# Optimization experiments

Measured on AMD Instinct MI355X. Metric: run time of the kernel, lower is better.

The kernel has to match this reference:

```python
import jax, jax.numpy as jnp
import numpy as np


def setup_inputs() -> dict:
    key = jax.random.key(0)
    ks = jax.random.split(key, 12)
    B, C, H, W = 8, 256, 64, 64
    inter = C // 8
    s = 0.05  # weight scale keeps q.k logits in a stable softmax range
    f32 = jnp.float32
    x = jax.random.normal(ks[0], (B, C, H, W), f32)
    Wq = jax.random.normal(ks[1], (inter, C), f32) * s
    bq = jnp.zeros((inter,), f32)
    Wk = jax.random.normal(ks[2], (inter, C), f32) * s
    bk = jnp.zeros((inter,), f32)
    Wv = jax.random.normal(ks[3], (C, C), f32) * s
    bv = jnp.zeros((C,), f32)
    gamma = jnp.full((1,), 0.5, f32)  # learnable residual scale (init 0 in torch; 0.5 exercises the path)
    Wg1 = jax.random.normal(ks[4], (inter, C), f32) * s
    bg1 = jnp.zeros((inter,), f32)
    Wg2 = jax.random.normal(ks[5], (C, inter), f32) * s
    bg2 = jnp.zeros((C,), f32)
    return {"x": x, "Wq": Wq, "bq": bq, "Wk": Wk, "bk": bk, "Wv": Wv, "bv": bv,
            "gamma": gamma, "Wg1": Wg1, "bg1": bg1, "Wg2": Wg2, "bg2": bg2}


def reference(x, Wq, bq, Wk, bk, Wv, bv, gamma, Wg1, bg1, Wg2, bg2):
    B, C, H, W = x.shape
    N = H * W
    xf = x.reshape(B, C, N)  # [B,C,N]
    # 1x1 convs == per-pixel linear projections
    q = jnp.einsum('oc,bcn->bon', Wq, xf) + bq[None, :, None]  # [B,inter,N]
    k = jnp.einsum('oc,bcn->bon', Wk, xf) + bk[None, :, None]  # [B,inter,N]
    v = jnp.einsum('oc,bcn->bon', Wv, xf) + bv[None, :, None]  # [B,C,N]
    # attention[b,n,m] = softmax_m( q[b,:,n] . k[b,:,m] )
    attn = jax.nn.softmax(jnp.einsum('bin,bim->bnm', q, k), axis=-1)  # [B,N,N]
    # out[b,c,n] = sum_m v[b,c,m] * attn[b,n,m]
    out = jnp.einsum('bcm,bnm->bcn', v, attn)  # [B,C,N]
    out = gamma[0] * out + xf
    # gated global pooling branch: GAP -> 1x1 conv -> ReLU -> 1x1 conv -> Sigmoid
    gp = xf.mean(axis=-1)  # [B,C]
    h = jax.nn.relu(jnp.einsum('oc,bc->bo', Wg1, gp) + bg1)  # [B,inter]
    ga = jax.nn.sigmoid(jnp.einsum('co,bo->bc', Wg2, h) + bg2)  # [B,C]
    out = out * ga[:, :, None] + out
    return out.reshape(B, C, H, W)
```

## Files before the change

kernel.cpp:

```cpp
#include <hip/hip_runtime.h>

typedef unsigned short u16;
typedef unsigned int   u32;
typedef short s16x4 __attribute__((ext_vector_type(4)));
typedef u16 u16x4 __attribute__((ext_vector_type(4)));
typedef u16 u16x8 __attribute__((ext_vector_type(8)));
typedef __bf16 bf16x8 __attribute__((ext_vector_type(8)));
typedef float f32x4 __attribute__((ext_vector_type(4)));

#define NB 8
#define NC 256
#define NI 32
#define NN 4096
#define LOG2E 1.4426950408889634f
#define POFF 64.0f

#define OW_Q   0
#define OB_Q   8192
#define OW_K   8224
#define OB_K   16416
#define OW_V   16448
#define OB_V   81984
#define OGAM   82240
#define OW_G1  82248
#define OB_G1  90440
#define OW_G2  90472
#define OB_G2  98664
#define WTOT   98920

__device__ __forceinline__ float bf2f(u16 v) {
    u32 u = ((u32)v) << 16;
    return __builtin_bit_cast(float, u);
}
__device__ __forceinline__ u16 f2bf(float f) {
    u32 u = __builtin_bit_cast(u32, f);
    u32 lsb = (u >> 16) & 1u;
    u += 0x7fffu + lsb;
    return (u16)(u >> 16);
}
__device__ __forceinline__ bool is_f32_mode(const void* graw) {
    return ((const u16*)graw)[0] == 0;
}

__global__ __launch_bounds__(256) void convert_kernel(
    const void* x,  const void* Wq, const void* bq, const void* Wk, const void* bk,
    const void* Wv, const void* bv, const void* gamma, const void* Wg1, const void* bg1,
    const void* Wg2, const void* bg2, float* __restrict__ xf, float* __restrict__ wbuf,
    u16* __restrict__ wbf, float* __restrict__ gp)
{
    bool f32m = is_f32_mode(gamma);
    int blk = blockIdx.x, t = threadIdx.x;
    if (blk < 2048) {
        int base = blk * 4096 + t * 16;
        float s = 0.f;
        if (f32m) {
            const float* xs = (const float*)x;
#pragma unroll
            for (int k = 0; k < 4; ++k) {
                f32x4 a = *(const f32x4*)(xs + base + k * 4);
                s += (a[0] + a[1]) + (a[2] + a[3]);
            }
        } else {
            const u16* xs = (const u16*)x;
#pragma unroll
            for (int k = 0; k < 2; ++k) {
                u16x8 a = *(const u16x8*)(xs + base + k * 8);
                f32x4 lo, hi;
#pragma unroll
                for (int j = 0; j < 4; ++j) { lo[j] = bf2f(a[j]); hi[j] = bf2f(a[4 + j]); }
                *(f32x4*)(xf + base + k * 8)     = lo;
                *(f32x4*)(xf + base + k * 8 + 4) = hi;
                s += (lo[0]+lo[1])+(lo[2]+lo[3]) + (hi[0]+hi[1])+(hi[2]+hi[3]);
            }
        }
#pragma unroll
        for (int off = 1; off <= 32; off <<= 1) s += __shfl_xor(s, off, 64);
        __shared__ float ws[4];
        if ((t & 63) == 0) ws[t >> 6] = s;
        __syncthreads();
        if (t == 0) gp[blk] = (ws[0] + ws[1] + ws[2] + ws[3]) * (1.0f / NN);
        return;
    }
    if (blk < 2080) {
        int tid = (blk - 2048) * 256 + t;
        const int off[12] = {OW_Q, OB_Q, OW_K, OB_K, OW_V, OB_V, OGAM, OW_G1, OB_G1, OW_G2, OB_G2, WTOT};
        const int len[11] = {8192, 32, 8192, 32, 65536, 256, 1, 8192, 32, 8192, 256};
        const void* srcs[11] = {Wq, bq, Wk, bk, Wv, bv, gamma, Wg1, bg1, Wg2, bg2};
        for (int w = tid; w < WTOT; w += 32 * 256) {
            int seg = 0;
#pragma unroll
            for (int i = 1; i < 11; ++i) if (w >= off[i]) seg = i;
            int idx = w - off[seg];
            float val = 0.f;
            if (idx < len[seg])
                val = f32m ? ((const float*)srcs[seg])[idx] : bf2f(((const u16*)srcs[seg])[idx]);
            wbuf[w] = val;
        }
        return;
    }
    int tid = (blk - 2080) * 256 + t;
    for (int w = tid; w < 320 * 256; w += 10 * 256) {
        int row = w >> 8, c = w & 255;
        const void* src; int idx; float scale = 1.f;
        if (row < 32)      { src = Wq; idx = row * 256 + c; scale = LOG2E; }
        else if (row < 64) { src = Wk; idx = (row - 32) * 256 + c; }
        else               { src = Wv; idx = (row - 64) * 256 + c; }
        float val = f32m ? ((const float*)src)[idx] : bf2f(((const u16*)src)[idx]);
        wbf[w] = f2bf(val * scale);
    }
}

__global__ __launch_bounds__(256) void proj_kernel(
    const void* xr, const float* __restrict__ xf, const void* graw,
    const float* __restrict__ wbuf, const u16* __restrict__ wbf,
    u16* __restrict__ qt, u16* __restrict__ kt, u16* __restrict__ v)
{
    __shared__ __attribute__((aligned(16))) u16 xs[64][264];

    const float* X = is_f32_mode(graw) ? (const float*)xr : xf;

    int t    = threadIdx.x;
    int lane = t & 63;
    int wave = t >> 6;
    int b    = blockIdx.x >> 6;
    int m0   = (blockIdx.x & 63) << 6;
    int l15  = lane & 15;
    int quad = lane >> 4;

    {
        const float* xb = X + (size_t)b * NC * NN + m0 + lane;
        int c0 = wave * 64;
#pragma unroll
        for (int ci = 0; ci < 64; ci += 4) {
            int c = c0 + ci;
            float a0 = xb[(size_t)(c    ) * NN];
            float a1 = xb[(size_t)(c + 1) * NN];
            float a2 = xb[(size_t)(c + 2) * NN];
            float a3 = xb[(size_t)(c + 3) * NN];
            u16x4 p4 = { f2bf(a0), f2bf(a1), f2bf(a2), f2bf(a3) };
            *(u16x4*)&xs[lane][c] = p4;
        }
    }
    __syncthreads();

    const f32x4 zero4 = {};
    f32x4 acc[5][4];
#pragma unroll
    for (int i = 0; i < 5; ++i)
#pragma unroll
        for (int mt = 0; mt < 4; ++mt) acc[i][mt] = zero4;

    int obase = wave * 80;
    const u16* wb = wbf + (size_t)(obase + l15) * 256 + quad * 8;

    bf16x8 af[5];
#pragma unroll
    for (int i = 0; i < 5; ++i)
        af[i] = *(const bf16x8*)(wb + (size_t)(i * 16) * 256);

#pragma unroll
    for (int kc = 0; kc < 8; ++kc) {
        bf16x8 afn[5], bfr[4];
        if (kc < 7) {
#pragma unroll
            for (int i = 0; i < 5; ++i)
                afn[i] = *(const bf16x8*)(wb + (size_t)(i * 16) * 256 + (kc + 1) * 32);
        }
#pragma unroll
        for (int mt = 0; mt < 4; ++mt)
            bfr[mt] = *(const bf16x8*)&xs[mt * 16 + l15][kc * 32 + quad * 8];
#pragma unroll
        for (int i = 0; i < 5; ++i)
#pragma unroll
            for (int mt = 0; mt < 4; ++mt)
                acc[i][mt] = __builtin_amdgcn_mfma_f32_16x16x32_bf16(af[i], bfr[mt], acc[i][mt], 0, 0, 0);
        if (kc < 7) {
#pragma unroll
            for (int i = 0; i < 5; ++i) af[i] = afn[i];
        }
    }

    __syncthreads();

    if (wave == 0) {
#pragma unroll
        for (int i = 0; i < 4; ++i) {
#pragma unroll
            for (int mt = 0; mt < 4; ++mt) {
                u16x4 tmp;
#pragma unroll
                for (int r = 0; r < 4; ++r) {
                    int o = i * 16 + quad * 4 + r;
                    float bias = (o < 32) ? LOG2E * wbuf[OB_Q + o] : wbuf[OB_K + o - 32];
                    tmp[r] = f2bf(acc[i][mt][r] + bias);
                }
                *(u16x4*)&xs[mt * 16 + l15][i * 16 + quad * 4] = tmp;
            }
        }
        int m = m0 + lane;
        u16* qrow = qt + (size_t)(b * NN + m) * NI;
        u16* krow = kt + (size_t)(b * NN + m) * NI;
#pragma unroll
        for (int j = 0; j < 4; ++j) *(u16x8*)(qrow + j * 8) = *(const u16x8*)&xs[lane][j * 8];
#pragma unroll
        for (int j = 0; j < 4; ++j) *(u16x8*)(krow + j * 8) = *(const u16x8*)&xs[lane][32 + j * 8];
#pragma unroll
        for (int mt = 0; mt < 4; ++mt) {
#pragma unroll
            for (int r = 0; r < 4; ++r) {
                int c = quad * 4 + r;
                v[(size_t)(b * NC + c) * NN + m0 + mt * 16 + l15] = f2bf(acc[4][mt][r] + wbuf[OB_V + c]);
            }
        }
    } else {
#pragma unroll
        for (int i = 0; i < 5; ++i) {
#pragma unroll
            for (int mt = 0; mt < 4; ++mt) {
#pragma unroll
                for (int r = 0; r < 4; ++r) {
                    int c = wave * 80 + i * 16 + quad * 4 + r - 64;
                    v[(size_t)(b * NC + c) * NN + m0 + mt * 16 + l15] = f2bf(acc[i][mt][r] + wbuf[OB_V + c]);
                }
            }
        }
    }
}

__global__ __launch_bounds__(256) void gate_kernel(
    const float* __restrict__ gp, const float* __restrict__ wbuf, float* __restrict__ gmul)
{
    int b = blockIdx.x;
    int t = threadIdx.x;
    __shared__ float gps[NC];
    __shared__ float hs[NI];
    gps[t] = gp[b * NC + t];
    __syncthreads();
    if (t < NI) {
        float a = wbuf[OB_G1 + t];
        for (int c = 0; c < NC; ++c) a += wbuf[OW_G1 + t * NC + c] * gps[c];
        hs[t] = a > 0.f ? a : 0.f;
    }
    __syncthreads();
    float a = wbuf[OB_G2 + t];
#pragma unroll
    for (int i = 0; i < NI; ++i) a += wbuf[OW_G2 + t * NI + i] * hs[i];
    float sig = 1.f / (1.f + __expf(-a));
    gmul[b * NC + t] = 1.f + sig;
}

__global__ __launch_bounds__(512, 4) void flash_kernel(
    const u16* __restrict__ qt, const u16* __restrict__ kt, const u16* __restrict__ v,
    const void* xr, const float* __restrict__ xf, const void* graw,
    const float* __restrict__ wbuf, const float* __restrict__ gmul, void* outp)
{
    __shared__ __attribute__((aligned(16))) u16 vs[2][NC][48];

    bool f32m = is_f32_mode(graw);
    const float* X = f32m ? (const float*)xr : xf;

    int t    = threadIdx.x;
    int lane = t & 63;
    int wave = t >> 6;
    int b    = blockIdx.x >> 6;
    int nblk = (blockIdx.x & 63) << 6;
    int n0   = nblk + (wave >> 2) * 32;
    int c0   = (wave & 3) * 64;
    int l15  = lane & 15;
    int quad = lane >> 4;

    const f32x4 zero4 = {};

    bf16x8 qf[2];
#pragma unroll
    for (int n16 = 0; n16 < 2; ++n16)
        qf[n16] = *(const bf16x8*)(qt + (size_t)(b * NN + n0 + n16 * 16 + l15) * NI + quad * 8);

    f32x4 acc[2][4];
#pragma unroll
    for (int n16 = 0; n16 < 2; ++n16)
#pragma unroll
        for (int ct = 0; ct < 4; ++ct) acc[n16][ct] = zero4;
    float psum[2] = {0.f, 0.f};

    int sc = t >> 2;
    int sm = (t & 3) * 8;
    const u16* vb0 = v + (size_t)(b * NC + sc) * NN + sm;
    const u16* vb1 = v + (size_t)(b * NC + sc + 128) * NN + sm;
    const u16* ktb = kt + (size_t)(b * NN + l15) * NI + quad * 8;

    u16x8 vr0 = *(const u16x8*)vb0;
    u16x8 vr1 = *(const u16x8*)vb1;
    *(u16x8*)&vs[0][sc][sm]       = vr0;
    *(u16x8*)&vs[0][sc + 128][sm] = vr1;
    bf16x8 ktf[2];
#pragma unroll
    for (int mt = 0; mt < 2; ++mt)
        ktf[mt] = *(const bf16x8*)(ktb + (size_t)(mt * 16) * NI);
    __syncthreads();

    for (int it = 0; it < NN / 32; ++it) {
        int cur  = it & 1;
        bool more = (it < NN / 32 - 1);
        int mnxt = it * 32 + 32;

        if (more) {
            vr0 = *(const u16x8*)(vb0 + mnxt);
            vr1 = *(const u16x8*)(vb1 + mnxt);
        }

        f32x4 sf[2][2];
#pragma unroll
        for (int mt = 0; mt < 2; ++mt)
#pragma unroll
            for (int n16 = 0; n16 < 2; ++n16)
                sf[n16][mt] = __builtin_amdgcn_mfma_f32_16x16x32_bf16(ktf[mt], qf[n16], zero4, 0, 0, 0);

        if (more) {
#pragma unroll
            for (int mt = 0; mt < 2; ++mt)
                ktf[mt] = *(const bf16x8*)(ktb + (size_t)(mnxt + mt * 16) * NI);
        }

        s16x4 pfr[2][2];
#pragma unroll
        for (int n16 = 0; n16 < 2; ++n16)
#pragma unroll
            for (int mt = 0; mt < 2; ++mt) {
                float p0 = __builtin_amdgcn_exp2f(sf[n16][mt][0] - POFF);
                float p1 = __builtin_amdgcn_exp2f(sf[n16][mt][1] - POFF);
                float p2 = __builtin_amdgcn_exp2f(sf[n16][mt][2] - POFF);
                float p3 = __builtin_amdgcn_exp2f(sf[n16][mt][3] - POFF);
                psum[n16] += (p0 + p1) + (p2 + p3);
                pfr[n16][mt] = s16x4{ (short)f2bf(p0), (short)f2bf(p1),
                                      (short)f2bf(p2), (short)f2bf(p3) };
            }

#pragma unroll
        for (int mt = 0; mt < 2; ++mt) {
            int mb = mt * 16 + quad * 4;
#pragma unroll
            for (int ct = 0; ct < 4; ++ct) {
                s16x4 va = *(const s16x4*)&vs[cur][c0 + ct * 16 + l15][mb];
#pragma unroll
                for (int n16 = 0; n16 < 2; ++n16)
                    acc[n16][ct] = __builtin_amdgcn_mfma_f32_16x16x16bf16_1k(va, pfr[n16][mt], acc[n16][ct], 0, 0, 0);
            }
        }

        if (more) {
            *(u16x8*)&vs[cur ^ 1][sc][sm]       = vr0;
            *(u16x8*)&vs[cur ^ 1][sc + 128][sm] = vr1;
        }
        __syncthreads();
    }

    float inv[2];
#pragma unroll
    for (int n16 = 0; n16 < 2; ++n16) {
        float s = psum[n16];
        s += __shfl_xor(s, 16, 64);
        s += __shfl_xor(s, 32, 64);
        inv[n16] = 1.f / s;
    }
    float gam = wbuf[OGAM];

#pragma unroll
    for (int n16 = 0; n16 < 2; ++n16) {
        int n = n0 + n16 * 16 + l15;
#pragma unroll
        for (int ct = 0; ct < 4; ++ct) {
            int cb = c0 + ct * 16 + quad * 4;
            f32x4 gm4 = *(const f32x4*)&gmul[b * NC + cb];
#pragma unroll
            for (int r = 0; r < 4; ++r) {
                size_t off = (size_t)(b * NC + cb + r) * NN + n;
                float val = (gam * acc[n16][ct][r] * inv[n16] + X[off]) * gm4[r];
                if (f32m) ((float*)outp)[off] = val;
                else      ((u16*)outp)[off]  = f2bf(val);
            }
        }
    }
}

extern "C" void kernel_launch(void* const* d_in, const int* in_sizes, int n_in,
                              void* d_out, int out_size, void* d_ws, size_t ws_size,
                              hipStream_t stream)
{
    const void* x     = d_in[0];
    const void* Wq    = d_in[1];
    const void* bq    = d_in[2];
    const void* Wk    = d_in[3];
    const void* bk    = d_in[4];
    const void* Wv    = d_in[5];
    const void* bvp   = d_in[6];
    const void* gamma = d_in[7];
    const void* Wg1   = d_in[8];
    const void* bg1   = d_in[9];
    const void* Wg2   = d_in[10];
    const void* bg2   = d_in[11];

    char* ws = (char*)d_ws;
    float* xf   = (float*)ws;
    float* wbuf = (float*)(ws + 33554432);
    u16*   qt   = (u16*)  (ws + 33951744);
    u16*   kt   = (u16*)  (ws + 36048896);
    u16*   v    = (u16*)  (ws + 38146048);
    float* gp   = (float*)(ws + 54923264);
    float* gmul = (float*)(ws + 54931456);
    u16*   wbf  = (u16*)  (ws + 54939648);

    convert_kernel<<<2090, 256, 0, stream>>>(x, Wq, bq, Wk, bk, Wv, bvp, gamma,
                                             Wg1, bg1, Wg2, bg2, xf, wbuf, wbf, gp);
    proj_kernel<<<NB * 64, 256, 0, stream>>>(x, xf, gamma, wbuf, wbf, qt, kt, v);
    gate_kernel<<<NB, 256, 0, stream>>>(gp, wbuf, gmul);
    flash_kernel<<<NB * 64, 512, 0, stream>>>(qt, kt, v, x, xf, gamma, wbuf, gmul, d_out);
}
```

Before: 321.2 us.

## Use 16x16x32 MFMA for PV with permlane-swapped P fragments and hardware bf16 packing

The PV product in the flash kernel now uses the wider 16x16x32 bf16 MFMA, issuing half as many MFMA instructions. The probability fragments are rearranged across lanes with permlane32/16 swaps so they match that MFMA's operand layout, and V tiles are read as 8-wide LDS loads with the row padding cut from 48 to 40. The softmax offset is folded into the QK MFMA accumulator init, row sums use packed f32x2 adds, and software bf16 rounding is replaced by v_cvt_pk_bf16_f32 everywhere. Blocks are also reordered so batch varies fastest. The lane permutes add work, and the new padding may change LDS bank conflicts.

```diff
diff --git a/kernel.cpp b/kernel.cpp
--- a/kernel.cpp
+++ b/kernel.cpp
@@ -7,6 +7,9 @@
 typedef u16 u16x8 __attribute__((ext_vector_type(8)));
 typedef __bf16 bf16x8 __attribute__((ext_vector_type(8)));
 typedef float f32x4 __attribute__((ext_vector_type(4)));
+typedef float f32x2 __attribute__((ext_vector_type(2)));
+typedef u32 u32x2v __attribute__((ext_vector_type(2)));
+typedef u32 u32x4v __attribute__((ext_vector_type(4)));
 
 #define NB 8
 #define NC 256
@@ -37,6 +40,42 @@
     u32 lsb = (u >> 16) & 1u;
     u += 0x7fffu + lsb;
     return (u16)(u >> 16);
+}
+__device__ __forceinline__ u32 cvtpk_bf16(float lo, float hi) {
+    u32 r;
+    asm("v_cvt_pk_bf16_f32 %0, %1, %2" : "=v"(r) : "v"(lo), "v"(hi));
+    return r;
+}
+__device__ __forceinline__ u16 f2bf_hw(float f) {
+    u32 r;
+    asm("v_cvt_pk_bf16_f32 %0, %1, %1" : "=v"(r) : "v"(f));
+    return (u16)r;
+}
+__device__ __forceinline__ void permswap32(u32& a, u32& b) {
+#if __has_builtin(__builtin_amdgcn_permlane32_swap)
+    auto r = __builtin_amdgcn_permlane32_swap(a, b, false, false);
+    a = (u32)r[0]; b = (u32)r[1];
+#else
+    int ln = (int)(threadIdx.x & 63);
+    u32 a2 = (u32)__shfl_xor((int)a, 32, 64);
+    u32 b2 = (u32)__shfl_xor((int)b, 32, 64);
+    u32 na = (ln < 32) ? a : b2;
+    u32 nb = (ln < 32) ? a2 : b;
+    a = na; b = nb;
+#endif
+}
+__device__ __forceinline__ void permswap16(u32& a, u32& b) {
+#if __has_builtin(__builtin_amdgcn_permlane16_swap)
+    auto r = __builtin_amdgcn_permlane16_swap(a, b, false, false);
+    a = (u32)r[0]; b = (u32)r[1];
+#else
+    int q = (int)((threadIdx.x >> 4) & 1);
+    u32 az = (u32)__shfl_xor((int)a, 16, 64);
+    u32 bz = (u32)__shfl_xor((int)b, 16, 64);
+    u32 na = q ? bz : a;
+    u32 nb = q ? b  : az;
+    a = na; b = nb;
+#endif
 }
 __device__ __forceinline__ bool is_f32_mode(const void* graw) {
     return ((const u16*)graw)[0] == 0;
@@ -137,8 +176,10 @@
             float a1 = xb[(size_t)(c + 1) * NN];
             float a2 = xb[(size_t)(c + 2) * NN];
             float a3 = xb[(size_t)(c + 3) * NN];
-            u16x4 p4 = { f2bf(a0), f2bf(a1), f2bf(a2), f2bf(a3) };
-            *(u16x4*)&xs[lane][c] = p4;
+            u32x2v p2;
+            p2.x = cvtpk_bf16(a0, a1);
+            p2.y = cvtpk_bf16(a2, a3);
+            *(u32x2v*)&xs[lane][c] = p2;
         }
     }
     __syncthreads();
@@ -187,14 +228,17 @@
         for (int i = 0; i < 4; ++i) {
 #pragma unroll
             for (int mt = 0; mt < 4; ++mt) {
-                u16x4 tmp;
+                float tv[4];
 #pragma unroll
                 for (int r = 0; r < 4; ++r) {
                     int o = i * 16 + quad * 4 + r;
                     float bias = (o < 32) ? LOG2E * wbuf[OB_Q + o] : wbuf[OB_K + o - 32];
-                    tmp[r] = f2bf(acc[i][mt][r] + bias);
+                    tv[r] = acc[i][mt][r] + bias;
                 }
-                *(u16x4*)&xs[mt * 16 + l15][i * 16 + quad * 4] = tmp;
+                u32x2v p2;
+                p2.x = cvtpk_bf16(tv[0], tv[1]);
+                p2.y = cvtpk_bf16(tv[2], tv[3]);
+                *(u32x2v*)&xs[mt * 16 + l15][i * 16 + quad * 4] = p2;
             }
         }
         int m = m0 + lane;
@@ -209,7 +253,7 @@
 #pragma unroll
             for (int r = 0; r < 4; ++r) {
                 int c = quad * 4 + r;
-                v[(size_t)(b * NC + c) * NN + m0 + mt * 16 + l15] = f2bf(acc[4][mt][r] + wbuf[OB_V + c]);
+                v[(size_t)(b * NC + c) * NN + m0 + mt * 16 + l15] = f2bf_hw(acc[4][mt][r] + wbuf[OB_V + c]);
             }
         }
     } else {
@@ -220,7 +264,7 @@
 #pragma unroll
                 for (int r = 0; r < 4; ++r) {
                     int c = wave * 80 + i * 16 + quad * 4 + r - 64;
-                    v[(size_t)(b * NC + c) * NN + m0 + mt * 16 + l15] = f2bf(acc[i][mt][r] + wbuf[OB_V + c]);
+                    v[(size_t)(b * NC + c) * NN + m0 + mt * 16 + l15] = f2bf_hw(acc[i][mt][r] + wbuf[OB_V + c]);
                 }
             }
         }
@@ -254,7 +298,7 @@
     const void* xr, const float* __restrict__ xf, const void* graw,
     const float* __restrict__ wbuf, const float* __restrict__ gmul, void* outp)
 {
-    __shared__ __attribute__((aligned(16))) u16 vs[2][NC][48];
+    __shared__ __attribute__((aligned(16))) u16 vs[2][NC][40];
 
     bool f32m = is_f32_mode(graw);
     const float* X = f32m ? (const float*)xr : xf;
@@ -262,14 +306,15 @@
     int t    = threadIdx.x;
     int lane = t & 63;
     int wave = t >> 6;
-    int b    = blockIdx.x >> 6;
-    int nblk = (blockIdx.x & 63) << 6;
+    int b    = blockIdx.x & 7;
+    int nblk = (blockIdx.x >> 3) << 6;
     int n0   = nblk + (wave >> 2) * 32;
     int c0   = (wave & 3) * 64;
     int l15  = lane & 15;
     int quad = lane >> 4;
 
     const f32x4 zero4 = {};
+    const f32x4 mneg  = {-POFF, -POFF, -POFF, -POFF};
 
     bf16x8 qf[2];
 #pragma unroll
@@ -281,7 +326,7 @@
     for (int n16 = 0; n16 < 2; ++n16)
 #pragma unroll
         for (int ct = 0; ct < 4; ++ct) acc[n16][ct] = zero4;
-    float psum[2] = {0.f, 0.f};
+    f32x2 psum2[2] = {};
 
     int sc = t >> 2;
     int sm = (t & 3) * 8;
@@ -314,7 +359,12 @@
         for (int mt = 0; mt < 2; ++mt)
 #pragma unroll
             for (int n16 = 0; n16 < 2; ++n16)
-                sf[n16][mt] = __builtin_amdgcn_mfma_f32_16x16x32_bf16(ktf[mt], qf[n16], zero4, 0, 0, 0);
+                sf[n16][mt] = __builtin_amdgcn_mfma_f32_16x16x32_bf16(ktf[mt], qf[n16], mneg, 0, 0, 0);
+
+        bf16x8 va8[4];
+#pragma unroll
+        for (int ct = 0; ct < 4; ++ct)
+            va8[ct] = *(const bf16x8*)&vs[cur][c0 + ct * 16 + l15][quad * 8];
 
         if (more) {
 #pragma unroll
@@ -322,31 +372,35 @@
                 ktf[mt] = *(const bf16x8*)(ktb + (size_t)(mnxt + mt * 16) * NI);
         }
 
-        s16x4 pfr[2][2];
-#pragma unroll
-        for (int n16 = 0; n16 < 2; ++n16)
-#pragma unroll
-            for (int mt = 0; mt < 2; ++mt) {
-                float p0 = __builtin_amdgcn_exp2f(sf[n16][mt][0] - POFF);
-                float p1 = __builtin_amdgcn_exp2f(sf[n16][mt][1] - POFF);
-                float p2 = __builtin_amdgcn_exp2f(sf[n16][mt][2] - POFF);
-                float p3 = __builtin_amdgcn_exp2f(sf[n16][mt][3] - POFF);
-                psum[n16] += (p0 + p1) + (p2 + p3);
-                pfr[n16][mt] = s16x4{ (short)f2bf(p0), (short)f2bf(p1),
-                                      (short)f2bf(p2), (short)f2bf(p3) };
-            }
-
-#pragma unroll
-        for (int mt = 0; mt < 2; ++mt) {
-            int mb = mt * 16 + quad * 4;
-#pragma unroll
-            for (int ct = 0; ct < 4; ++ct) {
-                s16x4 va = *(const s16x4*)&vs[cur][c0 + ct * 16 + l15][mb];
-#pragma unroll
-                for (int n16 = 0; n16 < 2; ++n16)
-                    acc[n16][ct] = __builtin_amdgcn_mfma_f32_16x16x16bf16_1k(va, pfr[n16][mt], acc[n16][ct], 0, 0, 0);
-            }
-        }
+        bf16x8 pfr8[2];
+#pragma unroll
+        for (int n16 = 0; n16 < 2; ++n16) {
+            float p[2][4];
+#pragma unroll
+            for (int mt = 0; mt < 2; ++mt)
+#pragma unroll
+                for (int r = 0; r < 4; ++r)
+                    p[mt][r] = __builtin_amdgcn_exp2f(sf[n16][mt][r]);
+            f32x2 t0; t0.x = p[0][0]; t0.y = p[0][1];
+            f32x2 t1; t1.x = p[0][2]; t1.y = p[0][3];
+            f32x2 t2; t2.x = p[1][0]; t2.y = p[1][1];
+            f32x2 t3; t3.x = p[1][2]; t3.y = p[1][3];
+            psum2[n16] += (t0 + t1) + (t2 + t3);
+            u32 A0 = cvtpk_bf16(p[0][0], p[0][1]);
+            u32 A1 = cvtpk_bf16(p[0][2], p[0][3]);
+            u32 B0 = cvtpk_bf16(p[1][0], p[1][1]);
+            u32 B1 = cvtpk_bf16(p[1][2], p[1][3]);
+            permswap32(A0, B0); permswap16(A0, B0);
+            permswap32(A1, B1); permswap16(A1, B1);
+            u32x4v f; f.x = A0; f.y = A1; f.z = B0; f.w = B1;
+            pfr8[n16] = __builtin_bit_cast(bf16x8, f);
+        }
+
+#pragma unroll
+        for (int ct = 0; ct < 4; ++ct)
+#pragma unroll
+            for (int n16 = 0; n16 < 2; ++n16)
+                acc[n16][ct] = __builtin_amdgcn_mfma_f32_16x16x32_bf16(va8[ct], pfr8[n16], acc[n16][ct], 0, 0, 0);
 
         if (more) {
             *(u16x8*)&vs[cur ^ 1][sc][sm]       = vr0;
@@ -358,7 +412,7 @@
     float inv[2];
 #pragma unroll
     for (int n16 = 0; n16 < 2; ++n16) {
-        float s = psum[n16];
+        float s = psum2[n16].x + psum2[n16].y;
         s += __shfl_xor(s, 16, 64);
         s += __shfl_xor(s, 32, 64);
         inv[n16] = 1.f / s;
@@ -377,7 +431,7 @@
                 size_t off = (size_t)(b * NC + cb + r) * NN + n;
                 float val = (gam * acc[n16][ct][r] * inv[n16] + X[off]) * gm4[r];
                 if (f32m) ((float*)outp)[off] = val;
-                else      ((u16*)outp)[off]  = f2bf(val);
+                else      ((u16*)outp)[off]  = f2bf_hw(val);
             }
         }
     }
```

Measured after the change: 280.6 us. 12.6% less time.
